# Performance work log

Hardware: AMD Instinct MI355X
Metric: run time of the kernel (lower is better)

The kernel has to match this reference:

```python
import jax, jax.numpy as jnp
import numpy as np

N_NODES = 100000
N_EDGES = 1600000
IN_CH = 128
HID = 128
OUT_CH = 10


def setup_inputs() -> dict:
    key = jax.random.key(0)
    ks = jax.random.split(key, 14)
    s_in = 1.0 / np.sqrt(IN_CH)
    s_h = 1.0 / np.sqrt(HID)
    return {
        "x0": jax.random.normal(ks[0], (N_NODES, IN_CH), jnp.float32),
        "edge_index": jax.random.randint(ks[1], (2, N_EDGES), 0, N_NODES, jnp.int32),
        "edge_weight": jax.random.uniform(ks[2], (N_EDGES,), jnp.float32),
        # GraphConv layer 1 (in -> hid): lin_rel (weight+bias) applied to aggregated msgs, lin_root (no bias)
        "W1_rel": jax.random.uniform(ks[3], (IN_CH, HID), jnp.float32, -s_in, s_in),
        "b1": jax.random.uniform(ks[4], (HID,), jnp.float32, -s_in, s_in),
        "W1_root": jax.random.uniform(ks[5], (IN_CH, HID), jnp.float32, -s_in, s_in),
        # GraphConv layer 2 (hid -> hid)
        "W2_rel": jax.random.uniform(ks[6], (HID, HID), jnp.float32, -s_h, s_h),
        "b2": jax.random.uniform(ks[7], (HID,), jnp.float32, -s_h, s_h),
        "W2_root": jax.random.uniform(ks[8], (HID, HID), jnp.float32, -s_h, s_h),
        # GraphConv layer 3 (hid -> hid)
        "W3_rel": jax.random.uniform(ks[9], (HID, HID), jnp.float32, -s_h, s_h),
        "b3": jax.random.uniform(ks[10], (HID,), jnp.float32, -s_h, s_h),
        "W3_root": jax.random.uniform(ks[11], (HID, HID), jnp.float32, -s_h, s_h),
        # classification head
        "W_lin": jax.random.uniform(ks[12], (HID, OUT_CH), jnp.float32, -s_h, s_h),
        "b_lin": jax.random.uniform(ks[13], (OUT_CH,), jnp.float32, -s_h, s_h),
    }


def _graph_conv(x, src, dst, ew, W_rel, b_rel, W_root):
    # message: x_j * w_e ; aggregate: scatter-add onto dst ; update: lin_rel(agg) + lin_root(x)
    msg = x[src] * ew[:, None]                                   # [E, C]
    agg = jax.ops.segment_sum(msg, dst, num_segments=x.shape[0])  # [N, C]
    return agg @ W_rel + b_rel + x @ W_root                      # [N, C']


def reference(x0, edge_index, edge_weight,
              W1_rel, b1, W1_root,
              W2_rel, b2, W2_root,
              W3_rel, b3, W3_root,
              W_lin, b_lin):
    src, dst = edge_index[0], edge_index[1]
    # dropout p=0.2 is identity in eval mode
    x1 = jax.nn.relu(_graph_conv(x0, src, dst, edge_weight, W1_rel, b1, W1_root))
    x2 = jax.nn.relu(_graph_conv(x1, src, dst, edge_weight, W2_rel, b2, W2_root))
    x3 = jax.nn.relu(_graph_conv(x2, src, dst, edge_weight, W3_rel, b3, W3_root))
    logits = x3 @ W_lin + b_lin
    return jax.nn.log_softmax(logits, axis=-1)
```

## Files before the change

kernel.cpp:

```cpp
#include <hip/hip_runtime.h>
#include <hip/hip_bf16.h>
#include <math.h>

#define C128 128
#define OUT_CH 10

typedef __attribute__((ext_vector_type(8))) short short8;
typedef __attribute__((ext_vector_type(4))) float f32x4;
typedef __attribute__((ext_vector_type(2))) float f32x2;
typedef __attribute__((ext_vector_type(4))) int i32x4;

__device__ __forceinline__ unsigned short f2bf(float f) {
    unsigned b = __float_as_uint(f);
    unsigned r = (b + 0x7FFF + ((b >> 16) & 1)) >> 16;
    return (unsigned short)r;
}
__device__ __forceinline__ float bf2f(unsigned short u) {
    return __uint_as_float(((unsigned)u) << 16);
}


#define NBMAX 400
#define BCAP  4608
#define P1K   4096

__global__ __launch_bounds__(512) void bin_kernel(
    const int* __restrict__ ei, const float* __restrict__ ew,
    int* __restrict__ gcur, uint2* __restrict__ bins, int E, int nb)
{
    __shared__ int cnt[NBMAX];
    __shared__ int pos[NBMAX];
    __shared__ int gbase[NBMAX];
    __shared__ int s[512];
    __shared__ int totalSh;
    __shared__ uint2 buf[P1K];

    const int t = threadIdx.x;
    const int e0 = blockIdx.x * P1K;

    for (int b = t; b < nb; b += 512) { cnt[b] = 0; pos[b] = 0; }
    __syncthreads();

    unsigned rec[8];
    int dstv[8];
    const int e = e0 + t * 8;
    if (e + 8 <= E) {
        i32x4 d0 = __builtin_nontemporal_load((const i32x4*)(ei + E + e));
        i32x4 d1 = __builtin_nontemporal_load((const i32x4*)(ei + E + e + 4));
        i32x4 s0 = __builtin_nontemporal_load((const i32x4*)(ei + e));
        i32x4 s1 = __builtin_nontemporal_load((const i32x4*)(ei + e + 4));
        f32x4 w0 = __builtin_nontemporal_load((const f32x4*)(ew + e));
        f32x4 w1 = __builtin_nontemporal_load((const f32x4*)(ew + e + 4));
        int dd[8] = {d0.x, d0.y, d0.z, d0.w, d1.x, d1.y, d1.z, d1.w};
        int ss[8] = {s0.x, s0.y, s0.z, s0.w, s1.x, s1.y, s1.z, s1.w};
        float ww[8] = {w0.x, w0.y, w0.z, w0.w, w1.x, w1.y, w1.z, w1.w};
#pragma unroll
        for (int j = 0; j < 8; ++j) {
            unsigned wb = __float_as_uint(ww[j]);
            unsigned r  = ((wb + 0x7FFF + ((wb >> 16) & 1)) >> 16) & 0x7FFFu;
            rec[j]  = (unsigned)ss[j] | (r << 17);
            dstv[j] = dd[j];
            atomicAdd(&cnt[dd[j] >> 8], 1);
        }
    } else {
#pragma unroll
        for (int j = 0; j < 8; ++j) {
            int ee = e + j;
            if (ee < E) {
                int dst = ei[E + ee];
                unsigned wb = __float_as_uint(ew[ee]);
                unsigned r  = ((wb + 0x7FFF + ((wb >> 16) & 1)) >> 16) & 0x7FFFu;
                rec[j]  = (unsigned)ei[ee] | (r << 17);
                dstv[j] = dst;
                atomicAdd(&cnt[dst >> 8], 1);
            } else {
                dstv[j] = -1;
            }
        }
    }
    __syncthreads();

    int c = (t < nb) ? cnt[t] : 0;
    s[t] = c;
    __syncthreads();
    for (int o = 1; o < 512; o <<= 1) {
        int u = (t >= o) ? s[t - o] : 0;
        __syncthreads();
        s[t] += u;
        __syncthreads();
    }
    if (t == nb - 1) totalSh = s[t];
    __syncthreads();

#pragma unroll
    for (int j = 0; j < 8; ++j) {
        if (dstv[j] >= 0) {
            int b = dstv[j] >> 8;
            int r = atomicAdd(&pos[b], 1);
            buf[s[b] - cnt[b] + r] = make_uint2(rec[j], (unsigned)dstv[j]);
        }
    }
    __syncthreads();

    if (t < nb) {
        int b = t + (int)((blockIdx.x * 131u) % (unsigned)nb);
        if (b >= nb) b -= nb;
        int cb = cnt[b];
        if (cb > 0) gbase[b] = atomicAdd(&gcur[b], cb);
    }
    __syncthreads();

    const int total = totalSh;
    for (int i = t; i < total; i += 512) {
        uint2 v = buf[i];
        int b = (int)(v.y >> 8);
        int dest = gbase[b] + (i - (s[b] - cnt[b]));
        if (dest < BCAP) bins[(size_t)b * BCAP + dest] = v;
    }
}

__global__ __launch_bounds__(512) void bucket_scan_kernel(
    const int* __restrict__ gcur, int* __restrict__ bbase,
    int* __restrict__ row_ptr, int nb, int N, int E)
{
    __shared__ int s[512];
    int t = threadIdx.x;
    int v = (t < nb) ? gcur[t] : 0;
    s[t] = v;
    __syncthreads();
    for (int o = 1; o < 512; o <<= 1) {
        int u = (t >= o) ? s[t - o] : 0;
        __syncthreads();
        s[t] += u;
        __syncthreads();
    }
    if (t < nb) bbase[t] = s[t] - v;
    if (t == 0) row_ptr[N] = E;
}

__global__ __launch_bounds__(256) void build_kernel(
    const uint2* __restrict__ bins, const int* __restrict__ gcur,
    const int* __restrict__ bbase, int* __restrict__ row_ptr,
    unsigned* __restrict__ csr, int N)
{
    __shared__ int rowCnt[256];
    __shared__ int rowOff[256];
    __shared__ int sc[256];
    __shared__ unsigned out[BCAP];

    const int b = blockIdx.x, t = threadIdx.x;
    int cnt = gcur[b];
    if (cnt > BCAP) cnt = BCAP;
    const int base = bbase[b];
    const uint2* mb = bins + (size_t)b * BCAP;

    rowCnt[t] = 0;
    __syncthreads();
    for (int i = t; i < cnt; i += 256) atomicAdd(&rowCnt[(int)(mb[i].y & 255u)], 1);
    __syncthreads();

    int v = rowCnt[t];
    sc[t] = v;
    __syncthreads();
    for (int o = 1; o < 256; o <<= 1) {
        int u = (t >= o) ? sc[t - o] : 0;
        __syncthreads();
        sc[t] += u;
        __syncthreads();
    }
    rowOff[t] = sc[t] - v;
    int idx = b * 256 + t;
    if (idx <= N) row_ptr[idx] = base + sc[t] - v;
    rowCnt[t] = 0;
    __syncthreads();

    for (int i = t; i < cnt; i += 256) {
        uint2 r = mb[i];
        int d = (int)(r.y & 255u);
        int k = atomicAdd(&rowCnt[d], 1);
        out[rowOff[d] + k] = r.x;
    }
    __syncthreads();

    for (int i = t; i < cnt; i += 256) csr[base + i] = out[i];
}


__global__ __launch_bounds__(256) void cvt_both_kernel(const float4* __restrict__ x,
                                                       ushort4* __restrict__ xb,
                                                       unsigned* __restrict__ xf8, int n4) {
    int i = blockIdx.x * blockDim.x + threadIdx.x;
    if (i < n4) {
        float4 v = x[i];
        ushort4 o;
        o.x = f2bf(v.x); o.y = f2bf(v.y); o.z = f2bf(v.z); o.w = f2bf(v.w);
        xb[i] = o;
        unsigned p = __builtin_amdgcn_cvt_pk_fp8_f32(v.x, v.y, 0, false);
        p = __builtin_amdgcn_cvt_pk_fp8_f32(v.z, v.w, p, true);
        xf8[i] = p;
    }
}


__global__ __launch_bounds__(256) void pack_w_kernel(const float* __restrict__ Wr,
                                                     const float* __restrict__ Wt,
                                                     unsigned short* __restrict__ Wp) {
    int idx = blockIdx.x * 256 + threadIdx.x;
    int j    = idx & 7;
    int n    = (idx >> 3) & 127;
    int quad = (idx >> 10) & 3;
    int ks   = idx >> 12;
    const float* W = (ks < 4) ? Wr : Wt;
    int k = (ks & 3) * 32 + quad * 8 + j;
    Wp[idx] = f2bf(W[(size_t)k * C128 + n]);
}


__global__ __launch_bounds__(256) void gather_fp8_kernel(
    const unsigned* __restrict__ xf8,
    const int* __restrict__ row_ptr,
    const unsigned* __restrict__ csr, unsigned short* __restrict__ aggb, int N)
{
    int node = blockIdx.x * 4 + (threadIdx.x >> 6);
    if (node >= N) return;
    int lane = threadIdx.x & 63;
    int g   = lane >> 4;
    int l16 = lane & 15;
    int i0  = row_ptr[node];
    int deg = row_ptr[node + 1] - i0;

    float acc[8];
#pragma unroll
    for (int j = 0; j < 8; ++j) acc[j] = 0.f;

    for (int base = 0; base < deg; base += 64) {
        int rem = deg - base; if (rem > 64) rem = 64;
        int rec = 0;
        if (base + lane < deg) rec = (int)csr[i0 + base + lane];

        int c = 0;
        for (; c + 16 <= rem; c += 16) {
            int s0 = __shfl(rec, c + g,      64);
            int s1 = __shfl(rec, c + 4 + g,  64);
            int s2 = __shfl(rec, c + 8 + g,  64);
            int s3 = __shfl(rec, c + 12 + g, 64);
            float w0 = __uint_as_float(((unsigned)s0 >> 17) << 16);
            float w1 = __uint_as_float(((unsigned)s1 >> 17) << 16);
            float w2 = __uint_as_float(((unsigned)s2 >> 17) << 16);
            float w3 = __uint_as_float(((unsigned)s3 >> 17) << 16);
            uint2 q0 = *(const uint2*)&xf8[(size_t)(s0 & 0x1FFFF) * 32 + l16 * 2];
            uint2 q1 = *(const uint2*)&xf8[(size_t)(s1 & 0x1FFFF) * 32 + l16 * 2];
            uint2 q2 = *(const uint2*)&xf8[(size_t)(s2 & 0x1FFFF) * 32 + l16 * 2];
            uint2 q3 = *(const uint2*)&xf8[(size_t)(s3 & 0x1FFFF) * 32 + l16 * 2];
#define ACCUM(q, w)                                                          \
            {                                                                \
                f32x2 a01 = __builtin_amdgcn_cvt_pk_f32_fp8((q).x, false);   \
                f32x2 a23 = __builtin_amdgcn_cvt_pk_f32_fp8((q).x, true);    \
                f32x2 a45 = __builtin_amdgcn_cvt_pk_f32_fp8((q).y, false);   \
                f32x2 a67 = __builtin_amdgcn_cvt_pk_f32_fp8((q).y, true);    \
                acc[0] += a01.x * (w); acc[1] += a01.y * (w);                \
                acc[2] += a23.x * (w); acc[3] += a23.y * (w);                \
                acc[4] += a45.x * (w); acc[5] += a45.y * (w);                \
                acc[6] += a67.x * (w); acc[7] += a67.y * (w);                \
            }
            ACCUM(q0, w0) ACCUM(q1, w1) ACCUM(q2, w2) ACCUM(q3, w3)
        }
        for (; c < rem; c += 4) {
            int idx = c + g;
            int im = idx & 63;
            int s = __shfl(rec, im, 64);
            float w = __uint_as_float(((unsigned)s >> 17) << 16);
            if (idx >= rem) w = 0.f;
            uint2 q = *(const uint2*)&xf8[(size_t)(s & 0x1FFFF) * 32 + l16 * 2];
            ACCUM(q, w)
        }
#undef ACCUM
    }

#pragma unroll
    for (int j = 0; j < 8; ++j) {
        acc[j] += __shfl_xor(acc[j], 16, 64);
        acc[j] += __shfl_xor(acc[j], 32, 64);
    }
    if (g == 0) {
        uint4 o;
        o.x = (unsigned)f2bf(acc[0]) | ((unsigned)f2bf(acc[1]) << 16);
        o.y = (unsigned)f2bf(acc[2]) | ((unsigned)f2bf(acc[3]) << 16);
        o.z = (unsigned)f2bf(acc[4]) | ((unsigned)f2bf(acc[5]) << 16);
        o.w = (unsigned)f2bf(acc[6]) | ((unsigned)f2bf(acc[7]) << 16);
        *(uint4*)&aggb[(size_t)node * C128 + l16 * 8] = o;
    }
}


#define A_STRIDE 40

__global__ __launch_bounds__(256) void gemm_mfma(
    const unsigned short* __restrict__ aggb, const unsigned short* __restrict__ xb,
    const unsigned short* __restrict__ Wp, const float* __restrict__ bias,
    unsigned short* __restrict__ outb, unsigned char* __restrict__ outf8, int N)
{
    __shared__ unsigned short WL[8 * 4 * 128 * 8];
    __shared__ unsigned short AL[64 * A_STRIDE];

    const int t = threadIdx.x;
    const int node0 = blockIdx.x * 64;
    const int w    = t >> 6;
    const int lane = t & 63;
    const int l15  = lane & 15;
    const int quad = lane >> 4;

#pragma unroll
    for (int i = 0; i < 16; ++i) {
        int slot = i * 256 + t;
        *(uint4*)&WL[slot * 8] = *(const uint4*)&Wp[slot * 8];
    }

    float bv[8];
#pragma unroll
    for (int nt = 0; nt < 8; ++nt) bv[nt] = bias[nt * 16 + l15];

    f32x4 acc[8];
#pragma unroll
    for (int nt = 0; nt < 8; ++nt) acc[nt] = (f32x4){0.f, 0.f, 0.f, 0.f};

    const int sr = t >> 2;
    const int sc = t & 3;
    const int srow = node0 + sr;

    for (int ks = 0; ks < 8; ++ks) {
        const unsigned short* Asrc = (ks < 4) ? aggb : xb;
        const int koff = (ks & 3) * 32;
        __syncthreads();
        uint4 av = make_uint4(0u, 0u, 0u, 0u);
        if (srow < N) av = *(const uint4*)&Asrc[(size_t)srow * C128 + koff + sc * 8];
        *(uint4*)&AL[sr * A_STRIDE + sc * 8] = av;
        __syncthreads();

        short8 a = *(const short8*)&AL[(w * 16 + l15) * A_STRIDE + quad * 8];
#pragma unroll
        for (int nt = 0; nt < 8; ++nt) {
            short8 b = *(const short8*)&WL[(((ks * 4 + quad) * 128) + nt * 16 + l15) * 8];
            acc[nt] = __builtin_amdgcn_mfma_f32_16x16x32_bf16(a, b, acc[nt], 0, 0, 0);
        }
    }

#pragma unroll
    for (int r = 0; r < 4; ++r) {
        int row = node0 + w * 16 + quad * 4 + r;
        if (row < N) {
#pragma unroll
            for (int nt = 0; nt < 8; ++nt) {
                float v = fmaxf(acc[nt][r] + bv[nt], 0.f);
                outb[(size_t)row * C128 + nt * 16 + l15] = f2bf(v);
                if (outf8) {
                    unsigned p8 = __builtin_amdgcn_cvt_pk_fp8_f32(v, 0.f, 0, false);
                    outf8[(size_t)row * C128 + nt * 16 + l15] = (unsigned char)(p8 & 0xff);
                }
            }
        }
    }
}


__global__ __launch_bounds__(256) void head_kernel(
    const unsigned short* __restrict__ x, const float* __restrict__ Wl,
    const float* __restrict__ bl, float* __restrict__ out, int N)
{
    int n = blockIdx.x * blockDim.x + threadIdx.x;
    if (n >= N) return;
    float acc[OUT_CH];
#pragma unroll
    for (int c = 0; c < OUT_CH; ++c) acc[c] = bl[c];
    const ushort4* row = (const ushort4*)(x + (size_t)n * C128);
#pragma unroll 4
    for (int kk = 0; kk < 32; ++kk) {
        ushort4 u = row[kk];
        float vx = bf2f(u.x), vy = bf2f(u.y), vz = bf2f(u.z), vw = bf2f(u.w);
        int k = kk * 4;
#pragma unroll
        for (int c = 0; c < OUT_CH; ++c) {
            acc[c] += vx * Wl[(k + 0) * OUT_CH + c]
                    + vy * Wl[(k + 1) * OUT_CH + c]
                    + vz * Wl[(k + 2) * OUT_CH + c]
                    + vw * Wl[(k + 3) * OUT_CH + c];
        }
    }
    float m = acc[0];
#pragma unroll
    for (int c = 1; c < OUT_CH; ++c) m = fmaxf(m, acc[c]);
    float s = 0.f;
#pragma unroll
    for (int c = 0; c < OUT_CH; ++c) s += __expf(acc[c] - m);
    float lse = m + __logf(s);
#pragma unroll
    for (int c = 0; c < OUT_CH; ++c) out[(size_t)n * OUT_CH + c] = acc[c] - lse;
}


extern "C" void kernel_launch(void* const* d_in, const int* in_sizes, int n_in,
                              void* d_out, int out_size, void* d_ws, size_t ws_size,
                              hipStream_t stream) {
    const float* x0   = (const float*)d_in[0];
    const int*   ei   = (const int*)  d_in[1];
    const float* ew   = (const float*)d_in[2];
    const float* W1r  = (const float*)d_in[3];
    const float* b1   = (const float*)d_in[4];
    const float* W1t  = (const float*)d_in[5];
    const float* W2r  = (const float*)d_in[6];
    const float* b2   = (const float*)d_in[7];
    const float* W2t  = (const float*)d_in[8];
    const float* W3r  = (const float*)d_in[9];
    const float* b3   = (const float*)d_in[10];
    const float* W3t  = (const float*)d_in[11];
    const float* Wlin = (const float*)d_in[12];
    const float* blin = (const float*)d_in[13];

    const int N = in_sizes[0] / C128;
    const int E = in_sizes[1] / 2;
    const int nb = (N + 255) >> 8;

    char* ws = (char*)d_ws;
    size_t off = 0;
    auto alloc = [&](size_t bytes) {
        void* p = ws + off;
        off = (off + bytes + 255) & ~(size_t)255;
        return p;
    };
    size_t bb = (size_t)N * C128 * sizeof(unsigned short);
    size_t fb = (size_t)N * C128;
    unsigned short* aggb = (unsigned short*)alloc(bb);
    unsigned short* xb0  = (unsigned short*)alloc(bb);
    unsigned short* xb1  = (unsigned short*)alloc(bb);
    unsigned char*  xf8  = (unsigned char*)alloc(fb);
    unsigned short* Wp1  = (unsigned short*)alloc(32768 * 2);
    unsigned short* Wp2  = (unsigned short*)alloc(32768 * 2);
    unsigned short* Wp3  = (unsigned short*)alloc(32768 * 2);
    unsigned* csr  = (unsigned*)alloc((size_t)E * 4);
    int* row_ptr   = (int*)alloc((size_t)(N + 2) * 4);
    uint2* bins    = (uint2*)alloc((size_t)nb * BCAP * 8);
    int* gcur      = (int*)alloc((size_t)nb * 4);
    int* bbase     = (int*)alloc((size_t)nb * 4);

    hipMemsetAsync(gcur, 0, (size_t)nb * sizeof(int), stream);
    bin_kernel<<<(E + P1K - 1) / P1K, 512, 0, stream>>>(ei, ew, gcur, bins, E, nb);
    bucket_scan_kernel<<<1, 512, 0, stream>>>(gcur, bbase, row_ptr, nb, N, E);
    build_kernel<<<nb, 256, 0, stream>>>(bins, gcur, bbase, row_ptr, csr, N);

    cvt_both_kernel<<<(N * C128 / 4 + 255) / 256, 256, 0, stream>>>(
        (const float4*)x0, (ushort4*)xb0, (unsigned*)xf8, N * C128 / 4);
    pack_w_kernel<<<128, 256, 0, stream>>>(W1r, W1t, Wp1);
    pack_w_kernel<<<128, 256, 0, stream>>>(W2r, W2t, Wp2);
    pack_w_kernel<<<128, 256, 0, stream>>>(W3r, W3t, Wp3);

    int gatherGrid = (N + 3) / 4;
    int gemmGrid   = (N + 63) / 64;

    gather_fp8_kernel<<<gatherGrid, 256, 0, stream>>>(
        (const unsigned*)xf8, row_ptr, csr, aggb, N);
    gemm_mfma<<<gemmGrid, 256, 0, stream>>>(aggb, xb0, Wp1, b1, xb1, xf8, N);
    gather_fp8_kernel<<<gatherGrid, 256, 0, stream>>>(
        (const unsigned*)xf8, row_ptr, csr, aggb, N);
    gemm_mfma<<<gemmGrid, 256, 0, stream>>>(aggb, xb1, Wp2, b2, xb0, xf8, N);
    gather_fp8_kernel<<<gatherGrid, 256, 0, stream>>>(
        (const unsigned*)xf8, row_ptr, csr, aggb, N);
    gemm_mfma<<<gemmGrid, 256, 0, stream>>>(aggb, xb0, Wp3, b3, xb1, nullptr, N);
    head_kernel<<<(N + 255) / 256, 256, 0, stream>>>(xb1, Wlin, blin, (float*)d_out, N);
}
```

Baseline: 389.1 us.

## Fuse neighbor gather and MFMA GEMM into one per-layer kernel

Merges the fp8 gather-aggregate kernel and the bf16 MFMA GEMM into a single kernel per layer. Each wavefront aggregates 16 nodes into shared memory and then runs the GEMM directly on them, which removes the aggb round trip through global memory and two launches per layer. Weights are now read straight from global memory instead of being staged in LDS, fp8 feature buffers are double-buffered so a layer never overwrites its own input, and packed f32x2 math is used in the accumulation. In exchange, gather and GEMM work is serialized inside each wave and per-wave load can be uneven for nodes of different degree.

```diff
diff --git a/kernel.cpp b/kernel.cpp
--- a/kernel.cpp
+++ b/kernel.cpp
@@ -216,138 +216,124 @@
 }
 
 
-__global__ __launch_bounds__(256) void gather_fp8_kernel(
+#define AGS 136
+
+__global__ __launch_bounds__(256, 5) void fused_layer(
     const unsigned* __restrict__ xf8,
     const int* __restrict__ row_ptr,
-    const unsigned* __restrict__ csr, unsigned short* __restrict__ aggb, int N)
-{
-    int node = blockIdx.x * 4 + (threadIdx.x >> 6);
-    if (node >= N) return;
-    int lane = threadIdx.x & 63;
-    int g   = lane >> 4;
-    int l16 = lane & 15;
-    int i0  = row_ptr[node];
-    int deg = row_ptr[node + 1] - i0;
-
-    float acc[8];
-#pragma unroll
-    for (int j = 0; j < 8; ++j) acc[j] = 0.f;
-
-    for (int base = 0; base < deg; base += 64) {
-        int rem = deg - base; if (rem > 64) rem = 64;
-        int rec = 0;
-        if (base + lane < deg) rec = (int)csr[i0 + base + lane];
-
-        int c = 0;
-        for (; c + 16 <= rem; c += 16) {
-            int s0 = __shfl(rec, c + g,      64);
-            int s1 = __shfl(rec, c + 4 + g,  64);
-            int s2 = __shfl(rec, c + 8 + g,  64);
-            int s3 = __shfl(rec, c + 12 + g, 64);
-            float w0 = __uint_as_float(((unsigned)s0 >> 17) << 16);
-            float w1 = __uint_as_float(((unsigned)s1 >> 17) << 16);
-            float w2 = __uint_as_float(((unsigned)s2 >> 17) << 16);
-            float w3 = __uint_as_float(((unsigned)s3 >> 17) << 16);
-            uint2 q0 = *(const uint2*)&xf8[(size_t)(s0 & 0x1FFFF) * 32 + l16 * 2];
-            uint2 q1 = *(const uint2*)&xf8[(size_t)(s1 & 0x1FFFF) * 32 + l16 * 2];
-            uint2 q2 = *(const uint2*)&xf8[(size_t)(s2 & 0x1FFFF) * 32 + l16 * 2];
-            uint2 q3 = *(const uint2*)&xf8[(size_t)(s3 & 0x1FFFF) * 32 + l16 * 2];
-#define ACCUM(q, w)                                                          \
-            {                                                                \
-                f32x2 a01 = __builtin_amdgcn_cvt_pk_f32_fp8((q).x, false);   \
-                f32x2 a23 = __builtin_amdgcn_cvt_pk_f32_fp8((q).x, true);    \
-                f32x2 a45 = __builtin_amdgcn_cvt_pk_f32_fp8((q).y, false);   \
-                f32x2 a67 = __builtin_amdgcn_cvt_pk_f32_fp8((q).y, true);    \
-                acc[0] += a01.x * (w); acc[1] += a01.y * (w);                \
-                acc[2] += a23.x * (w); acc[3] += a23.y * (w);                \
-                acc[4] += a45.x * (w); acc[5] += a45.y * (w);                \
-                acc[6] += a67.x * (w); acc[7] += a67.y * (w);                \
-            }
-            ACCUM(q0, w0) ACCUM(q1, w1) ACCUM(q2, w2) ACCUM(q3, w3)
-        }
-        for (; c < rem; c += 4) {
-            int idx = c + g;
-            int im = idx & 63;
-            int s = __shfl(rec, im, 64);
-            float w = __uint_as_float(((unsigned)s >> 17) << 16);
-            if (idx >= rem) w = 0.f;
-            uint2 q = *(const uint2*)&xf8[(size_t)(s & 0x1FFFF) * 32 + l16 * 2];
-            ACCUM(q, w)
-        }
-#undef ACCUM
-    }
-
-#pragma unroll
-    for (int j = 0; j < 8; ++j) {
-        acc[j] += __shfl_xor(acc[j], 16, 64);
-        acc[j] += __shfl_xor(acc[j], 32, 64);
-    }
-    if (g == 0) {
-        uint4 o;
-        o.x = (unsigned)f2bf(acc[0]) | ((unsigned)f2bf(acc[1]) << 16);
-        o.y = (unsigned)f2bf(acc[2]) | ((unsigned)f2bf(acc[3]) << 16);
-        o.z = (unsigned)f2bf(acc[4]) | ((unsigned)f2bf(acc[5]) << 16);
-        o.w = (unsigned)f2bf(acc[6]) | ((unsigned)f2bf(acc[7]) << 16);
-        *(uint4*)&aggb[(size_t)node * C128 + l16 * 8] = o;
-    }
-}
-
-
-#define A_STRIDE 40
-
-__global__ __launch_bounds__(256) void gemm_mfma(
-    const unsigned short* __restrict__ aggb, const unsigned short* __restrict__ xb,
+    const unsigned* __restrict__ csr,
+    const unsigned short* __restrict__ xb,
     const unsigned short* __restrict__ Wp, const float* __restrict__ bias,
     unsigned short* __restrict__ outb, unsigned char* __restrict__ outf8, int N)
 {
-    __shared__ unsigned short WL[8 * 4 * 128 * 8];
-    __shared__ unsigned short AL[64 * A_STRIDE];
+    __shared__ unsigned short AGL[4][16 * AGS];
 
     const int t = threadIdx.x;
-    const int node0 = blockIdx.x * 64;
     const int w    = t >> 6;
     const int lane = t & 63;
     const int l15  = lane & 15;
     const int quad = lane >> 4;
-
-#pragma unroll
+    const int wnode0 = blockIdx.x * 64 + w * 16;
+
+    int rrow = wnode0 + l15;
+    if (rrow >= N) rrow = 0;
+    short8 aroot[4];
+#pragma unroll
+    for (int k = 0; k < 4; ++k)
+        aroot[k] = *(const short8*)&xb[(size_t)rrow * C128 + k * 32 + quad * 8];
+
+    float bv[8];
+#pragma unroll
+    for (int nt = 0; nt < 8; ++nt) bv[nt] = bias[nt * 16 + l15];
+
     for (int i = 0; i < 16; ++i) {
-        int slot = i * 256 + t;
-        *(uint4*)&WL[slot * 8] = *(const uint4*)&Wp[slot * 8];
-    }
-
-    float bv[8];
-#pragma unroll
-    for (int nt = 0; nt < 8; ++nt) bv[nt] = bias[nt * 16 + l15];
+        int node = wnode0 + i;
+        int i0 = 0, deg = 0;
+        if (node < N) { i0 = row_ptr[node]; deg = row_ptr[node + 1] - i0; }
+
+        f32x2 acc2[4];
+#pragma unroll
+        for (int j = 0; j < 4; ++j) acc2[j] = (f32x2){0.f, 0.f};
+
+        for (int base = 0; base < deg; base += 64) {
+            int rem = deg - base; if (rem > 64) rem = 64;
+            int rec = 0;
+            if (base + lane < deg) rec = (int)csr[i0 + base + lane];
+
+            int c = 0;
+            for (; c + 16 <= rem; c += 16) {
+                int s0 = __shfl(rec, c + quad,      64);
+                int s1 = __shfl(rec, c + 4 + quad,  64);
+                int s2 = __shfl(rec, c + 8 + quad,  64);
+                int s3 = __shfl(rec, c + 12 + quad, 64);
+                float w0 = __uint_as_float(((unsigned)s0 >> 17) << 16);
+                float w1 = __uint_as_float(((unsigned)s1 >> 17) << 16);
+                float w2 = __uint_as_float(((unsigned)s2 >> 17) << 16);
+                float w3 = __uint_as_float(((unsigned)s3 >> 17) << 16);
+                uint2 q0 = *(const uint2*)&xf8[(size_t)(s0 & 0x1FFFF) * 32 + l15 * 2];
+                uint2 q1 = *(const uint2*)&xf8[(size_t)(s1 & 0x1FFFF) * 32 + l15 * 2];
+                uint2 q2 = *(const uint2*)&xf8[(size_t)(s2 & 0x1FFFF) * 32 + l15 * 2];
+                uint2 q3 = *(const uint2*)&xf8[(size_t)(s3 & 0x1FFFF) * 32 + l15 * 2];
+#define ACCUM(q, wv)                                                         \
+                {                                                            \
+                    f32x2 w2v = {(wv), (wv)};                                \
+                    acc2[0] += __builtin_amdgcn_cvt_pk_f32_fp8((q).x, false) * w2v; \
+                    acc2[1] += __builtin_amdgcn_cvt_pk_f32_fp8((q).x, true)  * w2v; \
+                    acc2[2] += __builtin_amdgcn_cvt_pk_f32_fp8((q).y, false) * w2v; \
+                    acc2[3] += __builtin_amdgcn_cvt_pk_f32_fp8((q).y, true)  * w2v; \
+                }
+                ACCUM(q0, w0) ACCUM(q1, w1) ACCUM(q2, w2) ACCUM(q3, w3)
+            }
+            for (; c < rem; c += 4) {
+                int idx = c + quad;
+                int im = idx & 63;
+                int s = __shfl(rec, im, 64);
+                float wv = __uint_as_float(((unsigned)s >> 17) << 16);
+                if (idx >= rem) wv = 0.f;
+                uint2 q = *(const uint2*)&xf8[(size_t)(s & 0x1FFFF) * 32 + l15 * 2];
+                ACCUM(q, wv)
+            }
+#undef ACCUM
+        }
+
+#pragma unroll
+        for (int j = 0; j < 4; ++j) {
+            acc2[j].x += __shfl_xor(acc2[j].x, 16, 64);
+            acc2[j].y += __shfl_xor(acc2[j].y, 16, 64);
+            acc2[j].x += __shfl_xor(acc2[j].x, 32, 64);
+            acc2[j].y += __shfl_xor(acc2[j].y, 32, 64);
+        }
+        if (quad == 0) {
+            uint4 o;
+            o.x = (unsigned)f2bf(acc2[0].x) | ((unsigned)f2bf(acc2[0].y) << 16);
+            o.y = (unsigned)f2bf(acc2[1].x) | ((unsigned)f2bf(acc2[1].y) << 16);
+            o.z = (unsigned)f2bf(acc2[2].x) | ((unsigned)f2bf(acc2[2].y) << 16);
+            o.w = (unsigned)f2bf(acc2[3].x) | ((unsigned)f2bf(acc2[3].y) << 16);
+            *(uint4*)&AGL[w][i * AGS + l15 * 8] = o;
+        }
+    }
 
     f32x4 acc[8];
 #pragma unroll
     for (int nt = 0; nt < 8; ++nt) acc[nt] = (f32x4){0.f, 0.f, 0.f, 0.f};
 
-    const int sr = t >> 2;
-    const int sc = t & 3;
-    const int srow = node0 + sr;
-
+#pragma unroll
     for (int ks = 0; ks < 8; ++ks) {
-        const unsigned short* Asrc = (ks < 4) ? aggb : xb;
-        const int koff = (ks & 3) * 32;
-        __syncthreads();
-        uint4 av = make_uint4(0u, 0u, 0u, 0u);
-        if (srow < N) av = *(const uint4*)&Asrc[(size_t)srow * C128 + koff + sc * 8];
-        *(uint4*)&AL[sr * A_STRIDE + sc * 8] = av;
-        __syncthreads();
-
-        short8 a = *(const short8*)&AL[(w * 16 + l15) * A_STRIDE + quad * 8];
+        short8 a;
+        if (ks < 4)
+            a = *(const short8*)&AGL[w][l15 * AGS + ks * 32 + quad * 8];
+        else
+            a = aroot[ks - 4];
 #pragma unroll
         for (int nt = 0; nt < 8; ++nt) {
-            short8 b = *(const short8*)&WL[(((ks * 4 + quad) * 128) + nt * 16 + l15) * 8];
+            short8 b = *(const short8*)&Wp[(((ks * 4 + quad) * 128) + nt * 16 + l15) * 8];
             acc[nt] = __builtin_amdgcn_mfma_f32_16x16x32_bf16(a, b, acc[nt], 0, 0, 0);
         }
     }
 
 #pragma unroll
     for (int r = 0; r < 4; ++r) {
-        int row = node0 + w * 16 + quad * 4 + r;
+        int row = wnode0 + quad * 4 + r;
         if (row < N) {
 #pragma unroll
             for (int nt = 0; nt < 8; ++nt) {
@@ -429,10 +415,10 @@
     };
     size_t bb = (size_t)N * C128 * sizeof(unsigned short);
     size_t fb = (size_t)N * C128;
-    unsigned short* aggb = (unsigned short*)alloc(bb);
     unsigned short* xb0  = (unsigned short*)alloc(bb);
     unsigned short* xb1  = (unsigned short*)alloc(bb);
-    unsigned char*  xf8  = (unsigned char*)alloc(fb);
+    unsigned char*  xf8a = (unsigned char*)alloc(fb);
+    unsigned char*  xf8b = (unsigned char*)alloc(fb);
     unsigned short* Wp1  = (unsigned short*)alloc(32768 * 2);
     unsigned short* Wp2  = (unsigned short*)alloc(32768 * 2);
     unsigned short* Wp3  = (unsigned short*)alloc(32768 * 2);
@@ -448,22 +434,18 @@
     build_kernel<<<nb, 256, 0, stream>>>(bins, gcur, bbase, row_ptr, csr, N);
 
     cvt_both_kernel<<<(N * C128 / 4 + 255) / 256, 256, 0, stream>>>(
-        (const float4*)x0, (ushort4*)xb0, (unsigned*)xf8, N * C128 / 4);
+        (const float4*)x0, (ushort4*)xb0, (unsigned*)xf8a, N * C128 / 4);
     pack_w_kernel<<<128, 256, 0, stream>>>(W1r, W1t, Wp1);
     pack_w_kernel<<<128, 256, 0, stream>>>(W2r, W2t, Wp2);
     pack_w_kernel<<<128, 256, 0, stream>>>(W3r, W3t, Wp3);
 
-    int gatherGrid = (N + 3) / 4;
-    int gemmGrid   = (N + 63) / 64;
-
-    gather_fp8_kernel<<<gatherGrid, 256, 0, stream>>>(
-        (const unsigned*)xf8, row_ptr, csr, aggb, N);
-    gemm_mfma<<<gemmGrid, 256, 0, stream>>>(aggb, xb0, Wp1, b1, xb1, xf8, N);
-    gather_fp8_kernel<<<gatherGrid, 256, 0, stream>>>(
-        (const unsigned*)xf8, row_ptr, csr, aggb, N);
-    gemm_mfma<<<gemmGrid, 256, 0, stream>>>(aggb, xb1, Wp2, b2, xb0, xf8, N);
-    gather_fp8_kernel<<<gatherGrid, 256, 0, stream>>>(
-        (const unsigned*)xf8, row_ptr, csr, aggb, N);
-    gemm_mfma<<<gemmGrid, 256, 0, stream>>>(aggb, xb0, Wp3, b3, xb1, nullptr, N);
+    const int fusedGrid = (N + 63) / 64;
+
+    fused_layer<<<fusedGrid, 256, 0, stream>>>(
+        (const unsigned*)xf8a, row_ptr, csr, xb0, Wp1, b1, xb1, xf8b, N);
+    fused_layer<<<fusedGrid, 256, 0, stream>>>(
+        (const unsigned*)xf8b, row_ptr, csr, xb1, Wp2, b2, xb0, xf8a, N);
+    fused_layer<<<fusedGrid, 256, 0, stream>>>(
+        (const unsigned*)xf8a, row_ptr, csr, xb0, Wp3, b3, xb1, nullptr, N);
     head_kernel<<<(N + 255) / 256, 256, 0, stream>>>(xb1, Wlin, blin, (float*)d_out, N);
 }
```

Result: slower. 443.3 us (+14.0%).

## Drop LDS staging in GEMM and pack gather accumulation into float2 ops

Applied to the files above, without the earlier changes.

The GEMM kernel no longer copies the packed weights and activation tiles into shared memory with per-step barriers. Each wave now loads its 16 rows of A fragments straight from global memory into registers and reads B fragments directly from global, relying on the cache since every block shares the same 64 KB of packed weights. This removes the LDS fill, the 16 block barriers and the LDS footprint, which can raise occupancy, but adds repeated global/L2 weight reads per wave. Separately, the gather kernel keeps its accumulators as float2 vectors so the FP8-decode multiply-adds can map to packed FMA instructions.

```diff
diff --git a/kernel.cpp b/kernel.cpp
--- a/kernel.cpp
+++ b/kernel.cpp
@@ -229,9 +229,9 @@
     int i0  = row_ptr[node];
     int deg = row_ptr[node + 1] - i0;
 
-    float acc[8];
-#pragma unroll
-    for (int j = 0; j < 8; ++j) acc[j] = 0.f;
+    f32x2 acc2[4];
+#pragma unroll
+    for (int j = 0; j < 4; ++j) acc2[j] = (f32x2){0.f, 0.f};
 
     for (int base = 0; base < deg; base += 64) {
         int rem = deg - base; if (rem > 64) rem = 64;
@@ -252,16 +252,13 @@
             uint2 q1 = *(const uint2*)&xf8[(size_t)(s1 & 0x1FFFF) * 32 + l16 * 2];
             uint2 q2 = *(const uint2*)&xf8[(size_t)(s2 & 0x1FFFF) * 32 + l16 * 2];
             uint2 q3 = *(const uint2*)&xf8[(size_t)(s3 & 0x1FFFF) * 32 + l16 * 2];
-#define ACCUM(q, w)                                                          \
+#define ACCUM(q, wv)                                                         \
             {                                                                \
-                f32x2 a01 = __builtin_amdgcn_cvt_pk_f32_fp8((q).x, false);   \
-                f32x2 a23 = __builtin_amdgcn_cvt_pk_f32_fp8((q).x, true);    \
-                f32x2 a45 = __builtin_amdgcn_cvt_pk_f32_fp8((q).y, false);   \
-                f32x2 a67 = __builtin_amdgcn_cvt_pk_f32_fp8((q).y, true);    \
-                acc[0] += a01.x * (w); acc[1] += a01.y * (w);                \
-                acc[2] += a23.x * (w); acc[3] += a23.y * (w);                \
-                acc[4] += a45.x * (w); acc[5] += a45.y * (w);                \
-                acc[6] += a67.x * (w); acc[7] += a67.y * (w);                \
+                f32x2 w2v = {(wv), (wv)};                                    \
+                acc2[0] += __builtin_amdgcn_cvt_pk_f32_fp8((q).x, false) * w2v; \
+                acc2[1] += __builtin_amdgcn_cvt_pk_f32_fp8((q).x, true)  * w2v; \
+                acc2[2] += __builtin_amdgcn_cvt_pk_f32_fp8((q).y, false) * w2v; \
+                acc2[3] += __builtin_amdgcn_cvt_pk_f32_fp8((q).y, true)  * w2v; \
             }
             ACCUM(q0, w0) ACCUM(q1, w1) ACCUM(q2, w2) ACCUM(q3, w3)
         }
@@ -269,52 +266,54 @@
             int idx = c + g;
             int im = idx & 63;
             int s = __shfl(rec, im, 64);
-            float w = __uint_as_float(((unsigned)s >> 17) << 16);
-            if (idx >= rem) w = 0.f;
+            float wv = __uint_as_float(((unsigned)s >> 17) << 16);
+            if (idx >= rem) wv = 0.f;
             uint2 q = *(const uint2*)&xf8[(size_t)(s & 0x1FFFF) * 32 + l16 * 2];
-            ACCUM(q, w)
+            ACCUM(q, wv)
         }
 #undef ACCUM
     }
 
 #pragma unroll
-    for (int j = 0; j < 8; ++j) {
-        acc[j] += __shfl_xor(acc[j], 16, 64);
-        acc[j] += __shfl_xor(acc[j], 32, 64);
+    for (int j = 0; j < 4; ++j) {
+        acc2[j].x += __shfl_xor(acc2[j].x, 16, 64);
+        acc2[j].y += __shfl_xor(acc2[j].y, 16, 64);
+        acc2[j].x += __shfl_xor(acc2[j].x, 32, 64);
+        acc2[j].y += __shfl_xor(acc2[j].y, 32, 64);
     }
     if (g == 0) {
         uint4 o;
-        o.x = (unsigned)f2bf(acc[0]) | ((unsigned)f2bf(acc[1]) << 16);
-        o.y = (unsigned)f2bf(acc[2]) | ((unsigned)f2bf(acc[3]) << 16);
-        o.z = (unsigned)f2bf(acc[4]) | ((unsigned)f2bf(acc[5]) << 16);
-        o.w = (unsigned)f2bf(acc[6]) | ((unsigned)f2bf(acc[7]) << 16);
+        o.x = (unsigned)f2bf(acc2[0].x) | ((unsigned)f2bf(acc2[0].y) << 16);
+        o.y = (unsigned)f2bf(acc2[1].x) | ((unsigned)f2bf(acc2[1].y) << 16);
+        o.z = (unsigned)f2bf(acc2[2].x) | ((unsigned)f2bf(acc2[2].y) << 16);
+        o.w = (unsigned)f2bf(acc2[3].x) | ((unsigned)f2bf(acc2[3].y) << 16);
         *(uint4*)&aggb[(size_t)node * C128 + l16 * 8] = o;
     }
 }
 
 
-#define A_STRIDE 40
-
-__global__ __launch_bounds__(256) void gemm_mfma(
+__global__ __launch_bounds__(256) void gemm_slim(
     const unsigned short* __restrict__ aggb, const unsigned short* __restrict__ xb,
     const unsigned short* __restrict__ Wp, const float* __restrict__ bias,
     unsigned short* __restrict__ outb, unsigned char* __restrict__ outf8, int N)
 {
-    __shared__ unsigned short WL[8 * 4 * 128 * 8];
-    __shared__ unsigned short AL[64 * A_STRIDE];
-
     const int t = threadIdx.x;
-    const int node0 = blockIdx.x * 64;
     const int w    = t >> 6;
     const int lane = t & 63;
     const int l15  = lane & 15;
     const int quad = lane >> 4;
-
-#pragma unroll
-    for (int i = 0; i < 16; ++i) {
-        int slot = i * 256 + t;
-        *(uint4*)&WL[slot * 8] = *(const uint4*)&Wp[slot * 8];
-    }
+    const int wnode0 = blockIdx.x * 64 + w * 16;
+
+    int arow = wnode0 + l15;
+    if (arow >= N) arow = N - 1;
+
+    short8 a[8];
+#pragma unroll
+    for (int k = 0; k < 4; ++k)
+        a[k] = *(const short8*)&aggb[(size_t)arow * C128 + k * 32 + quad * 8];
+#pragma unroll
+    for (int k = 0; k < 4; ++k)
+        a[4 + k] = *(const short8*)&xb[(size_t)arow * C128 + k * 32 + quad * 8];
 
     float bv[8];
 #pragma unroll
@@ -324,30 +323,18 @@
 #pragma unroll
     for (int nt = 0; nt < 8; ++nt) acc[nt] = (f32x4){0.f, 0.f, 0.f, 0.f};
 
-    const int sr = t >> 2;
-    const int sc = t & 3;
-    const int srow = node0 + sr;
-
+#pragma unroll
     for (int ks = 0; ks < 8; ++ks) {
-        const unsigned short* Asrc = (ks < 4) ? aggb : xb;
-        const int koff = (ks & 3) * 32;
-        __syncthreads();
-        uint4 av = make_uint4(0u, 0u, 0u, 0u);
-        if (srow < N) av = *(const uint4*)&Asrc[(size_t)srow * C128 + koff + sc * 8];
-        *(uint4*)&AL[sr * A_STRIDE + sc * 8] = av;
-        __syncthreads();
-
-        short8 a = *(const short8*)&AL[(w * 16 + l15) * A_STRIDE + quad * 8];
 #pragma unroll
         for (int nt = 0; nt < 8; ++nt) {
-            short8 b = *(const short8*)&WL[(((ks * 4 + quad) * 128) + nt * 16 + l15) * 8];
-            acc[nt] = __builtin_amdgcn_mfma_f32_16x16x32_bf16(a, b, acc[nt], 0, 0, 0);
+            short8 b = *(const short8*)&Wp[(((ks * 4 + quad) * 128) + nt * 16 + l15) * 8];
+            acc[nt] = __builtin_amdgcn_mfma_f32_16x16x32_bf16(a[ks], b, acc[nt], 0, 0, 0);
         }
     }
 
 #pragma unroll
     for (int r = 0; r < 4; ++r) {
-        int row = node0 + w * 16 + quad * 4 + r;
+        int row = wnode0 + quad * 4 + r;
         if (row < N) {
 #pragma unroll
             for (int nt = 0; nt < 8; ++nt) {
@@ -458,12 +445,12 @@
 
     gather_fp8_kernel<<<gatherGrid, 256, 0, stream>>>(
         (const unsigned*)xf8, row_ptr, csr, aggb, N);
-    gemm_mfma<<<gemmGrid, 256, 0, stream>>>(aggb, xb0, Wp1, b1, xb1, xf8, N);
+    gemm_slim<<<gemmGrid, 256, 0, stream>>>(aggb, xb0, Wp1, b1, xb1, xf8, N);
     gather_fp8_kernel<<<gatherGrid, 256, 0, stream>>>(
         (const unsigned*)xf8, row_ptr, csr, aggb, N);
-    gemm_mfma<<<gemmGrid, 256, 0, stream>>>(aggb, xb1, Wp2, b2, xb0, xf8, N);
+    gemm_slim<<<gemmGrid, 256, 0, stream>>>(aggb, xb1, Wp2, b2, xb0, xf8, N);
     gather_fp8_kernel<<<gatherGrid, 256, 0, stream>>>(
         (const unsigned*)xf8, row_ptr, csr, aggb, N);
-    gemm_mfma<<<gemmGrid, 256, 0, stream>>>(aggb, xb0, Wp3, b3, xb1, nullptr, N);
+    gemm_slim<<<gemmGrid, 256, 0, stream>>>(aggb, xb0, Wp3, b3, xb1, nullptr, N);
     head_kernel<<<(N + 255) / 256, 256, 0, stream>>>(xb1, Wlin, blin, (float*)d_out, N);
 }
```

After: 388.1 us. Within noise of the previous version (-0.2%).
